# Optimization experiments

Hardware: AMD Instinct MI355X
Metric: run time of the kernel (lower is better)

## Reference

```python
import jax, jax.numpy as jnp
import numpy as np

H = 1024
V_IN = 32000
V_OUT = 32000
T = 2048
BOS, EOS = 1, 2
MAX_STEPS = 50


def setup_inputs() -> dict:
    key = jax.random.key(0)
    ks = jax.random.split(key, 10)
    def n(k, shape, scale=0.05):
        return jax.random.normal(k, shape, jnp.float32) * scale
    return {
        "src_ids": jax.random.randint(ks[0], (T,), 3, V_IN),
        "embed_input": n(ks[1], (V_IN, H), 0.1),
        "We_ih": n(ks[2], (4 * H, H)),
        "We_hh": n(ks[3], (4 * H, H)),
        "be": jnp.zeros((4 * H,), jnp.float32),
        "embed_target": n(ks[4], (V_OUT, H), 0.1),
        "Wd_ih": n(ks[5], (4 * H, H)),
        "Wd_hh": n(ks[6], (4 * H, H)),
        "bd": jnp.zeros((4 * H,), jnp.float32),
        "W_attn": n(ks[7], (H, 2 * H)),
        "b_attn": jnp.zeros((H,), jnp.float32),
        "W_out": n(ks[8], (V_OUT, H)),
        "b_out": jnp.zeros((V_OUT,), jnp.float32),
    }


def _lstm_cell(x, h, c, W_ih, W_hh, b):
    # torch LSTMCell gate order: i, f, g, o (b = b_ih + b_hh folded)
    g = W_ih @ x + W_hh @ h + b  # [4H]
    i, f, gg, o = jnp.split(g, 4)
    i = jax.nn.sigmoid(i)
    f = jax.nn.sigmoid(f)
    o = jax.nn.sigmoid(o)
    gg = jnp.tanh(gg)
    c2 = f * c + i * gg
    return o * jnp.tanh(c2), c2


def reference(src_ids, embed_input, We_ih, We_hh, be, embed_target,
              Wd_ih, Wd_hh, bd, W_attn, b_attn, W_out, b_out):
    # ---- encoder: token-wise LSTMCell scan (batch 1, state squeezed to [H]) ----
    emb = embed_input[src_ids]  # [T, H] gather (unknown-word fallback handled by in-range ids)
    h0 = jnp.zeros((H,), jnp.float32)

    def enc_step(carry, x):
        h, c = carry
        h, c = _lstm_cell(x, h, c, We_ih, We_hh, be)
        return (h, c), h

    (hT, cT), hs = jax.lax.scan(enc_step, (h0, h0), emb)  # hs: [T, H]

    # ---- greedy decoder with dot attention, fixed 50 steps + done mask ----
    def dec_step(carry, _):
        wid, ht, ct, done = carry
        x = embed_target[wid]
        ht, ct = _lstm_cell(x, ht, ct, Wd_ih, Wd_hh, bd)
        a = jax.nn.softmax(hs @ ht)          # [T] attention over encoder states
        d = a @ hs                           # [H] context
        ht_new = jnp.tanh(W_attn @ jnp.concatenate([d, ht]) + b_attn)
        logits = W_out @ ht_new + b_out      # [V_OUT]; softmax before argmax is monotone -> skip
        nid = jnp.argmax(logits).astype(wid.dtype)
        tok = jnp.where(done, 0, nid)        # pad after <eos>
        out_logits = jnp.where(done, 0.0, logits)
        done2 = done | (nid == EOS)
        return (nid, ht, ct, done2), (tok, out_logits)

    init = (jnp.asarray(BOS, src_ids.dtype), hT, cT, jnp.asarray(False))
    _, (tokens, logits) = jax.lax.scan(dec_step, init, None, length=MAX_STEPS)
    return tokens, logits  # [50], [50, V_OUT]
```

## Files before the change

kernel.cpp:

```cpp
#include <hip/hip_runtime.h>
#include <math.h>

#define HD     1024
#define TLEN   2048
#define G4H    4096
#define VOUTN  32000
#define NSTEP  50
#define BOS_ID 1
#define EOS_ID 2

#define NBLK 256
#define NTHR 256
#define JPB  (HD / NBLK)
#define TPB  (TLEN / NBLK)
#define RPB  (VOUTN / NBLK)

#define ENBLK 64
#define ENTHR 1024
#define EJPB  (HD / ENBLK)

#define SENTINEL 0xFFFFFFFFu

#define OFF_GX   ((size_t)0)
#define OFF_HS   (OFF_GX + (size_t)TLEN * G4H)
#define OFF_HD   (OFF_HS + (size_t)(TLEN + 1) * HD)
#define OFF_SC   (OFF_HD + 2 * HD)
#define OFF_DC   (OFF_SC + TLEN)
#define OFF_HTN  (OFF_DC + HD)
#define OFF_BMV  (OFF_HTN + HD)
#define OFF_BMI  (OFF_BMV + NBLK)
#define OFF_CT   (OFF_BMI + NBLK)
#define OFF_ST   (OFF_CT + HD)

#define DEV_SCOPE __HIP_MEMORY_SCOPE_AGENT

__device__ __forceinline__ float dload(const float* p) {
    return __hip_atomic_load(p, __ATOMIC_RELAXED, DEV_SCOPE);
}
__device__ __forceinline__ void dstore(float* p, float v) {
    __hip_atomic_store(p, v, __ATOMIC_RELAXED, DEV_SCOPE);
}

__global__ __launch_bounds__(256) void fill_sentinel(float* __restrict__ hsrow1)
{
    const size_t i = ((size_t)blockIdx.x * 256 + threadIdx.x) * 4;
    uint4 v = make_uint4(SENTINEL, SENTINEL, SENTINEL, SENTINEL);
    *(uint4*)(hsrow1 + i) = v;
}

__global__ __launch_bounds__(256) void gx_gemm(
    const int* __restrict__ src_ids,
    const float* __restrict__ emb,
    const float* __restrict__ Wih,
    const float* __restrict__ be,
    float* __restrict__ Gx)
{
    __shared__ float As[128][17];
    __shared__ float Bs[128][17];
    __shared__ int   sid[128];

    const int tid = threadIdx.x;
    const int t0 = blockIdx.x * 128;
    const int r0 = blockIdx.y * 128;

    if (tid < 128) sid[tid] = src_ids[t0 + tid];
    __syncthreads();

    const int tx = tid & 15;
    const int ty = tid >> 4;
    const int lrow = tid >> 1;
    const int lk   = (tid & 1) * 8;

    float acc[8][8];
#pragma unroll
    for (int i = 0; i < 8; ++i)
#pragma unroll
        for (int j = 0; j < 8; ++j) acc[i][j] = 0.f;

    for (int k0 = 0; k0 < HD; k0 += 16) {
        {
            const float* xa = emb + (size_t)sid[lrow] * HD + k0 + lk;
            float4 v0 = *(const float4*)xa;
            float4 v1 = *(const float4*)(xa + 4);
            As[lrow][lk + 0] = v0.x; As[lrow][lk + 1] = v0.y;
            As[lrow][lk + 2] = v0.z; As[lrow][lk + 3] = v0.w;
            As[lrow][lk + 4] = v1.x; As[lrow][lk + 5] = v1.y;
            As[lrow][lk + 6] = v1.z; As[lrow][lk + 7] = v1.w;
            const float* wb = Wih + (size_t)(r0 + lrow) * HD + k0 + lk;
            float4 w0 = *(const float4*)wb;
            float4 w1 = *(const float4*)(wb + 4);
            Bs[lrow][lk + 0] = w0.x; Bs[lrow][lk + 1] = w0.y;
            Bs[lrow][lk + 2] = w0.z; Bs[lrow][lk + 3] = w0.w;
            Bs[lrow][lk + 4] = w1.x; Bs[lrow][lk + 5] = w1.y;
            Bs[lrow][lk + 6] = w1.z; Bs[lrow][lk + 7] = w1.w;
        }
        __syncthreads();
#pragma unroll
        for (int kk = 0; kk < 16; ++kk) {
            float a[8], bv[8];
#pragma unroll
            for (int i = 0; i < 8; ++i) a[i]  = As[ty * 8 + i][kk];
#pragma unroll
            for (int j = 0; j < 8; ++j) bv[j] = Bs[tx * 8 + j][kk];
#pragma unroll
            for (int i = 0; i < 8; ++i)
#pragma unroll
                for (int j = 0; j < 8; ++j)
                    acc[i][j] = fmaf(a[i], bv[j], acc[i][j]);
        }
        __syncthreads();
    }

    float bev[8];
#pragma unroll
    for (int j = 0; j < 8; ++j) bev[j] = be[r0 + tx * 8 + j];
#pragma unroll
    for (int i = 0; i < 8; ++i) {
        const int t = t0 + ty * 8 + i;
        float* dst = Gx + (size_t)t * G4H + r0 + tx * 8;
#pragma unroll
        for (int j = 0; j < 8; ++j) dst[j] = acc[i][j] + bev[j];
    }
}

__global__ __launch_bounds__(1024, 4) void enc_kernel(
    const float* __restrict__ Whh,
    const float* __restrict__ Gx,
    float* __restrict__ wsf)
{
    float* hs   = wsf + OFF_HS;
    float* hd   = wsf + OFF_HD;
    float* cdec = wsf + OFF_CT;
    int*   st   = (int*)(wsf + OFF_ST);

    const int b    = blockIdx.x;
    const int tid  = threadIdx.x;
    const int w    = tid >> 6;
    const int lane = tid & 63;
    const int j0   = b * EJPB;
    const int g    = w >> 2;
    const int e0   = (w & 3) * 4;

    __shared__ float bufH[HD];
    __shared__ float g_s[64];
    __shared__ float c_s[EJPB];

    float wreg[4][16];
#pragma unroll
    for (int d = 0; d < 4; ++d) {
        const int grow = g * HD + j0 + e0 + d;
        const float* src = Whh + (size_t)grow * HD + lane;
#pragma unroll
        for (int q = 0; q < 16; ++q) wreg[d][q] = src[q * 64];
    }

    if (tid < EJPB) c_s[tid] = 0.f;

    for (int t = 0; t < TLEN; ++t) {
        {
            const float* src = hs + (size_t)t * HD + tid;
            float v = dload(src);
            while (__float_as_uint(v) == SENTINEL) {
                __builtin_amdgcn_s_sleep(1);
                v = dload(src);
            }
            bufH[tid] = v;
        }
        __syncthreads();

        float acc[4];
#pragma unroll
        for (int d = 0; d < 4; ++d) {
            float a = 0.f;
#pragma unroll
            for (int q = 0; q < 16; ++q)
                a = fmaf(wreg[d][q], bufH[q * 64 + lane], a);
#pragma unroll
            for (int off = 32; off > 0; off >>= 1) a += __shfl_down(a, off);
            acc[d] = a;
        }
        if (lane == 0) {
#pragma unroll
            for (int d = 0; d < 4; ++d) g_s[g * 16 + e0 + d] = acc[d];
        }
        __syncthreads();

        if (tid < EJPB) {
            const int j = j0 + tid;
            const float* gx = Gx + (size_t)t * G4H;
            const float gi = g_s[tid]      + gx[0 * HD + j];
            const float gf = g_s[16 + tid] + gx[1 * HD + j];
            const float gg = g_s[32 + tid] + gx[2 * HD + j];
            const float go = g_s[48 + tid] + gx[3 * HD + j];
            const float i_ = 1.f / (1.f + expf(-gi));
            const float f_ = 1.f / (1.f + expf(-gf));
            const float o_ = 1.f / (1.f + expf(-go));
            const float g2 = tanhf(gg);
            const float c2 = f_ * c_s[tid] + i_ * g2;
            c_s[tid] = c2;
            dstore(hs + (size_t)(t + 1) * HD + j, o_ * tanhf(c2));
        }
    }

    if (tid < EJPB) {
        cdec[j0 + tid] = c_s[tid];
        hd[j0 + tid]   = hs[(size_t)TLEN * HD + j0 + tid];
    }
    if (b == 0 && tid == 0) st[0] = BOS_ID;
}


__global__ __launch_bounds__(256) void k_gates(
    const float* __restrict__ embT,
    const float* __restrict__ Wdih,
    const float* __restrict__ Wdhh,
    const float* __restrict__ bdv,
    float* __restrict__ wsf, int s)
{
    float* hd   = wsf + OFF_HD;
    float* cdec = wsf + OFF_CT;
    const int* st = (const int*)(wsf + OFF_ST);

    const int b    = blockIdx.x;
    const int tid  = threadIdx.x;
    const int w    = tid >> 6;
    const int lane = tid & 63;
    const int j0   = b * JPB;

    const float* hcur = hd + (s & 1) * HD;
    float*       hnxt = hd + ((s + 1) & 1) * HD;

    __shared__ float bufAB[2 * HD];
    __shared__ float g_s[4 * JPB];
    const float4* buf4 = (const float4*)bufAB;

    const int widv = st[s] & 0xFFFF;
    const float* x = embT + (size_t)widv * HD;
    for (int i = tid; i < HD; i += NTHR) {
        bufAB[i]      = x[i];
        bufAB[HD + i] = hcur[i];
    }
    __syncthreads();

#pragma unroll
    for (int d = 0; d < 4; ++d) {
        const int grow = w * HD + j0 + d;
        const float4* wi4 = (const float4*)(Wdih + (size_t)grow * HD);
        const float4* wh4 = (const float4*)(Wdhh + (size_t)grow * HD);
        float4 a4 = make_float4(0.f, 0.f, 0.f, 0.f);
#pragma unroll
        for (int q = 0; q < 4; ++q) {
            float4 wv = wi4[q * 64 + lane], xv = buf4[q * 64 + lane];
            a4.x = fmaf(wv.x, xv.x, a4.x); a4.y = fmaf(wv.y, xv.y, a4.y);
            a4.z = fmaf(wv.z, xv.z, a4.z); a4.w = fmaf(wv.w, xv.w, a4.w);
            float4 wv2 = wh4[q * 64 + lane], hv = buf4[256 + q * 64 + lane];
            a4.x = fmaf(wv2.x, hv.x, a4.x); a4.y = fmaf(wv2.y, hv.y, a4.y);
            a4.z = fmaf(wv2.z, hv.z, a4.z); a4.w = fmaf(wv2.w, hv.w, a4.w);
        }
        float a = (a4.x + a4.y) + (a4.z + a4.w);
#pragma unroll
        for (int off = 32; off > 0; off >>= 1) a += __shfl_down(a, off);
        if (lane == 0) g_s[w * 4 + d] = a;
    }
    __syncthreads();

    if (tid < JPB) {
        const int j = j0 + tid;
        const float gi = g_s[0 * 4 + tid] + bdv[0 * HD + j];
        const float gf = g_s[1 * 4 + tid] + bdv[1 * HD + j];
        const float gg = g_s[2 * 4 + tid] + bdv[2 * HD + j];
        const float go = g_s[3 * 4 + tid] + bdv[3 * HD + j];
        const float i_ = 1.f / (1.f + expf(-gi));
        const float f_ = 1.f / (1.f + expf(-gf));
        const float o_ = 1.f / (1.f + expf(-go));
        const float g2 = tanhf(gg);
        const float c2 = f_ * cdec[j] + i_ * g2;
        cdec[j] = c2;
        hnxt[j] = o_ * tanhf(c2);
    }
}

__global__ __launch_bounds__(256) void k_scores(float* __restrict__ wsf, int s)
{
    const float* hs = wsf + OFF_HS;
    const float* hnxt = wsf + OFF_HD + (size_t)((s + 1) & 1) * HD;
    float* sc = wsf + OFF_SC;

    const int b    = blockIdx.x;
    const int tid  = threadIdx.x;
    const int w    = tid >> 6;
    const int lane = tid & 63;

    __shared__ float bufH[HD];
    const float4* buf4 = (const float4*)bufH;
    for (int i = tid; i < HD; i += NTHR) bufH[i] = hnxt[i];
    __syncthreads();

#pragma unroll
    for (int d = 0; d < 2; ++d) {
        const int t = b * TPB + w * 2 + d;
        const float4* hr4 = (const float4*)(hs + (size_t)(t + 1) * HD);
        float4 a4 = make_float4(0.f, 0.f, 0.f, 0.f);
#pragma unroll
        for (int q = 0; q < 4; ++q) {
            float4 hv = hr4[q * 64 + lane], bv = buf4[q * 64 + lane];
            a4.x = fmaf(hv.x, bv.x, a4.x); a4.y = fmaf(hv.y, bv.y, a4.y);
            a4.z = fmaf(hv.z, bv.z, a4.z); a4.w = fmaf(hv.w, bv.w, a4.w);
        }
        float a = (a4.x + a4.y) + (a4.z + a4.w);
#pragma unroll
        for (int off = 32; off > 0; off >>= 1) a += __shfl_down(a, off);
        if (lane == 0) sc[t] = a;
    }
}

__global__ __launch_bounds__(256) void k_ctx(float* __restrict__ wsf)
{
    const float* hs = wsf + OFF_HS;
    const float* sc = wsf + OFF_SC;
    float* dctx = wsf + OFF_DC;

    const int b    = blockIdx.x;
    const int tid  = threadIdx.x;
    const int w    = tid >> 6;
    const int lane = tid & 63;
    const int j0   = b * JPB;

    __shared__ float sc_s[TLEN];
    __shared__ float red[NTHR];

    for (int t = tid; t < TLEN; t += NTHR) sc_s[t] = sc[t];
    __syncthreads();

    float lm = -INFINITY;
    for (int t = tid; t < TLEN; t += NTHR) lm = fmaxf(lm, sc_s[t]);
    red[tid] = lm; __syncthreads();
    for (int s2 = NTHR / 2; s2 > 0; s2 >>= 1) {
        if (tid < s2) red[tid] = fmaxf(red[tid], red[tid + s2]);
        __syncthreads();
    }
    const float m = red[0]; __syncthreads();
    float lz = 0.f;
    for (int t = tid; t < TLEN; t += NTHR) lz += expf(sc_s[t] - m);
    red[tid] = lz; __syncthreads();
    for (int s2 = NTHR / 2; s2 > 0; s2 >>= 1) {
        if (tid < s2) red[tid] += red[tid + s2];
        __syncthreads();
    }
    const float Zi = 1.f / red[0]; __syncthreads();

    const int j = j0 + w;
    float a = 0.f;
#pragma unroll
    for (int it = 0; it < TLEN / 64; ++it) {
        const int t = lane + it * 64;
        const float wt = expf(sc_s[t] - m) * Zi;
        a = fmaf(wt, hs[(size_t)(t + 1) * HD + j], a);
    }
#pragma unroll
    for (int off = 32; off > 0; off >>= 1) a += __shfl_down(a, off);
    if (lane == 0) dctx[j] = a;
}

__global__ __launch_bounds__(256) void k_attn(
    const float* __restrict__ Wattn,
    const float* __restrict__ battn,
    float* __restrict__ wsf, int s)
{
    const float* dctx = wsf + OFF_DC;
    const float* hnxt = wsf + OFF_HD + (size_t)((s + 1) & 1) * HD;
    float* htn = wsf + OFF_HTN;

    const int b    = blockIdx.x;
    const int tid  = threadIdx.x;
    const int w    = tid >> 6;
    const int lane = tid & 63;
    const int j0   = b * JPB;

    __shared__ float bufAB[2 * HD];
    const float4* buf4 = (const float4*)bufAB;
    for (int i = tid; i < HD; i += NTHR) {
        bufAB[i]      = dctx[i];
        bufAB[HD + i] = hnxt[i];
    }
    __syncthreads();

    const int j = j0 + w;
    const float4* wr4 = (const float4*)(Wattn + (size_t)j * (2 * HD));
    float4 a4 = make_float4(0.f, 0.f, 0.f, 0.f);
#pragma unroll
    for (int q = 0; q < 8; ++q) {
        float4 wv = wr4[q * 64 + lane], bv = buf4[q * 64 + lane];
        a4.x = fmaf(wv.x, bv.x, a4.x); a4.y = fmaf(wv.y, bv.y, a4.y);
        a4.z = fmaf(wv.z, bv.z, a4.z); a4.w = fmaf(wv.w, bv.w, a4.w);
    }
    float a = (a4.x + a4.y) + (a4.z + a4.w);
#pragma unroll
    for (int off = 32; off > 0; off >>= 1) a += __shfl_down(a, off);
    if (lane == 0) htn[j] = tanhf(a + battn[j]);
}

__global__ __launch_bounds__(256) void k_logits(
    const float* __restrict__ Wout,
    const float* __restrict__ bout,
    float* __restrict__ wsf,
    float* __restrict__ out, int s)
{
    const float* htn = wsf + OFF_HTN;
    float* bmv = wsf + OFF_BMV;
    int*   bmi = (int*)(wsf + OFF_BMI);
    const int* st = (const int*)(wsf + OFF_ST);

    const int b    = blockIdx.x;
    const int tid  = threadIdx.x;
    const int w    = tid >> 6;
    const int lane = tid & 63;

    __shared__ float bufH[HD];
    __shared__ float red[4];
    __shared__ int   redi[4];
    const float4* buf4 = (const float4*)bufH;

    const int donev = (st[s] >> 16) & 1;
    for (int i = tid; i < HD; i += NTHR) bufH[i] = htn[i];
    __syncthreads();

    const int r0b = b * RPB;
    const int rbeg = r0b + w * 32;
    const int rend = min(r0b + RPB, rbeg + 32);
    float bv = -INFINITY; int bi = 0x7fffffff;
    for (int r = rbeg; r < rend; r += 2) {
        const int two = (r + 1 < rend);
        const float4* w0 = (const float4*)(Wout + (size_t)r * HD);
        const float4* w1 = (const float4*)(Wout + (size_t)(r + two) * HD);
        float4 a04 = make_float4(0.f, 0.f, 0.f, 0.f);
        float4 a14 = make_float4(0.f, 0.f, 0.f, 0.f);
#pragma unroll
        for (int q = 0; q < 4; ++q) {
            float4 hv = buf4[q * 64 + lane];
            float4 x0 = w0[q * 64 + lane];
            float4 x1 = w1[q * 64 + lane];
            a04.x = fmaf(x0.x, hv.x, a04.x); a04.y = fmaf(x0.y, hv.y, a04.y);
            a04.z = fmaf(x0.z, hv.z, a04.z); a04.w = fmaf(x0.w, hv.w, a04.w);
            a14.x = fmaf(x1.x, hv.x, a14.x); a14.y = fmaf(x1.y, hv.y, a14.y);
            a14.z = fmaf(x1.z, hv.z, a14.z); a14.w = fmaf(x1.w, hv.w, a14.w);
        }
        float a0 = (a04.x + a04.y) + (a04.z + a04.w);
        float a1 = (a14.x + a14.y) + (a14.z + a14.w);
#pragma unroll
        for (int off = 32; off > 0; off >>= 1) {
            a0 += __shfl_down(a0, off);
            a1 += __shfl_down(a1, off);
        }
        if (lane == 0) {
            a0 += bout[r];
            out[NSTEP + (size_t)s * VOUTN + r] = donev ? 0.f : a0;
            if (a0 > bv) { bv = a0; bi = r; }
            if (two) {
                a1 += bout[r + 1];
                out[NSTEP + (size_t)s * VOUTN + r + 1] = donev ? 0.f : a1;
                if (a1 > bv) { bv = a1; bi = r + 1; }
            }
        }
    }
    if (lane == 0) { red[w] = bv; redi[w] = bi; }
    __syncthreads();
    if (tid == 0) {
        float v = red[0]; int ii = redi[0];
#pragma unroll
        for (int q = 1; q < 4; ++q)
            if (red[q] > v || (red[q] == v && redi[q] < ii)) { v = red[q]; ii = redi[q]; }
        bmv[b] = v; bmi[b] = ii;
    }
}

__global__ __launch_bounds__(256) void k_amax(
    float* __restrict__ wsf, float* __restrict__ out, int s)
{
    const float* bmv = wsf + OFF_BMV;
    const int*   bmi = (const int*)(wsf + OFF_BMI);
    int* st = (int*)(wsf + OFF_ST);

    const int tid = threadIdx.x;
    __shared__ float red[NTHR];
    __shared__ int   redi[NTHR];

    red[tid] = bmv[tid]; redi[tid] = bmi[tid];
    __syncthreads();
    for (int s2 = NTHR / 2; s2 > 0; s2 >>= 1) {
        if (tid < s2) {
            if (red[tid + s2] > red[tid] ||
                (red[tid + s2] == red[tid] && redi[tid + s2] < redi[tid])) {
                red[tid] = red[tid + s2]; redi[tid] = redi[tid + s2];
            }
        }
        __syncthreads();
    }
    if (tid == 0) {
        const int nid = redi[0];
        const int donev = (st[s] >> 16) & 1;
        out[s] = donev ? 0.f : (float)nid;
        const int done2 = donev | (nid == EOS_ID);
        st[s + 1] = (done2 << 16) | nid;
    }
}

extern "C" void kernel_launch(void* const* d_in, const int* in_sizes, int n_in,
                              void* d_out, int out_size, void* d_ws, size_t ws_size,
                              hipStream_t stream) {
    (void)in_sizes; (void)n_in; (void)out_size; (void)ws_size;
    const int*   src_ids = (const int*)  d_in[0];
    const float* emb_in  = (const float*)d_in[1];
    const float* We_ih   = (const float*)d_in[2];
    const float* We_hh   = (const float*)d_in[3];
    const float* be      = (const float*)d_in[4];
    const float* emb_tgt = (const float*)d_in[5];
    const float* Wd_ih   = (const float*)d_in[6];
    const float* Wd_hh   = (const float*)d_in[7];
    const float* bd      = (const float*)d_in[8];
    const float* W_attn  = (const float*)d_in[9];
    const float* b_attn  = (const float*)d_in[10];
    const float* W_out   = (const float*)d_in[11];
    const float* b_out   = (const float*)d_in[12];

    float* outp = (float*)d_out;
    float* wsf  = (float*)d_ws;

    hipMemsetAsync(wsf + OFF_HS, 0, HD * sizeof(float), stream);
    fill_sentinel<<<TLEN, 256, 0, stream>>>(wsf + OFF_HS + HD);

    dim3 g1(TLEN / 128, G4H / 128);
    gx_gemm<<<g1, 256, 0, stream>>>(src_ids, emb_in, We_ih, be, wsf + OFF_GX);

    {
        const float* a_Whh = We_hh;
        const float* a_Gx  = wsf + OFF_GX;
        float* a_ws  = wsf;
        void* args[] = { &a_Whh, &a_Gx, &a_ws };
        hipLaunchCooperativeKernel(reinterpret_cast<void*>(enc_kernel),
                                   dim3(ENBLK), dim3(ENTHR), args, 0, stream);
    }

    for (int s = 0; s < NSTEP; ++s) {
        k_gates <<<NBLK, NTHR, 0, stream>>>(emb_tgt, Wd_ih, Wd_hh, bd, wsf, s);
        k_scores<<<NBLK, NTHR, 0, stream>>>(wsf, s);
        k_ctx   <<<NBLK, NTHR, 0, stream>>>(wsf);
        k_attn  <<<NBLK, NTHR, 0, stream>>>(W_attn, b_attn, wsf, s);
        k_logits<<<NBLK, NTHR, 0, stream>>>(W_out, b_out, wsf, outp, s);
        k_amax  <<<1,    NTHR, 0, stream>>>(wsf, outp, s);
    }
}
```

Before: 10.30 ms.

## Fuse argmax into gates kernel, transpose encoder states, widen logits grid

The per-step single-block argmax kernel is removed. Every gates block now redoes the final argmax reduction over the logits partials, and block 0 writes the token and done state. The encoder states are transposed once after the encoder so the context reduction reads contiguous rows, and the logits kernel is spread over 500 blocks with a fixed 16 rows per wave. The encoder kernel also prefetches its input-gate slice into shared memory, and the softmax uses fast exp. This trades 50 kernel launches and strided reads for redundant reductions and an extra 8MB buffer.

```diff
diff --git a/kernel.cpp b/kernel.cpp
--- a/kernel.cpp
+++ b/kernel.cpp
@@ -1,4 +1,5 @@
 #include <hip/hip_runtime.h>
+#include <hip/hip_cooperative_groups.h>
 #include <math.h>
 
 #define HD     1024
@@ -9,11 +10,12 @@
 #define BOS_ID 1
 #define EOS_ID 2
 
-#define NBLK 256
-#define NTHR 256
-#define JPB  (HD / NBLK)
-#define TPB  (TLEN / NBLK)
-#define RPB  (VOUTN / NBLK)
+#define NBLK   256
+#define NTHR   256
+#define JPB    (HD / NBLK)
+#define TPB    (TLEN / NBLK)
+#define NBLK_L 500
+#define RPW_L  16
 
 #define ENBLK 64
 #define ENTHR 1024
@@ -28,9 +30,11 @@
 #define OFF_DC   (OFF_SC + TLEN)
 #define OFF_HTN  (OFF_DC + HD)
 #define OFF_BMV  (OFF_HTN + HD)
-#define OFF_BMI  (OFF_BMV + NBLK)
-#define OFF_CT   (OFF_BMI + NBLK)
+#define OFF_BMI  (OFF_BMV + 512)
+#define OFF_CT   (OFF_BMI + 512)
 #define OFF_ST   (OFF_CT + HD)
+#define OFF_HST  (OFF_ST + 64)
+#define WS_NEED_HST ((OFF_HST + (size_t)HD * TLEN) * sizeof(float))
 
 #define DEV_SCOPE __HIP_MEMORY_SCOPE_AGENT
 
@@ -144,6 +148,7 @@
     __shared__ float bufH[HD];
     __shared__ float g_s[64];
     __shared__ float c_s[EJPB];
+    __shared__ float gxbuf[64];
 
     float wreg[4][16];
 #pragma unroll
@@ -168,6 +173,13 @@
         }
         __syncthreads();
 
+        if (tid >= 64 && tid < 128) {
+            const int idx = tid - 64;
+            const int gg2 = idx >> 4;
+            const int ee  = idx & 15;
+            gxbuf[idx] = Gx[(size_t)t * G4H + gg2 * HD + j0 + ee];
+        }
+
         float acc[4];
 #pragma unroll
         for (int d = 0; d < 4; ++d) {
@@ -187,11 +199,10 @@
 
         if (tid < EJPB) {
             const int j = j0 + tid;
-            const float* gx = Gx + (size_t)t * G4H;
-            const float gi = g_s[tid]      + gx[0 * HD + j];
-            const float gf = g_s[16 + tid] + gx[1 * HD + j];
-            const float gg = g_s[32 + tid] + gx[2 * HD + j];
-            const float go = g_s[48 + tid] + gx[3 * HD + j];
+            const float gi = g_s[tid]      + gxbuf[tid];
+            const float gf = g_s[16 + tid] + gxbuf[16 + tid];
+            const float gg = g_s[32 + tid] + gxbuf[32 + tid];
+            const float go = g_s[48 + tid] + gxbuf[48 + tid];
             const float i_ = 1.f / (1.f + expf(-gi));
             const float f_ = 1.f / (1.f + expf(-gf));
             const float o_ = 1.f / (1.f + expf(-go));
@@ -209,17 +220,40 @@
     if (b == 0 && tid == 0) st[0] = BOS_ID;
 }
 
+__global__ __launch_bounds__(256) void k_transpose(
+    const float* __restrict__ hs, float* __restrict__ hsT)
+{
+    __shared__ float tile[32][33];
+    const int t0  = blockIdx.x * 32;
+    const int j0b = blockIdx.y * 32;
+    const int tx  = threadIdx.x & 31;
+    const int ty  = threadIdx.x >> 5;
+#pragma unroll
+    for (int k = 0; k < 4; ++k) {
+        const int trow = t0 + ty + k * 8;
+        tile[ty + k * 8][tx] = hs[(size_t)(trow + 1) * HD + j0b + tx];
+    }
+    __syncthreads();
+#pragma unroll
+    for (int k = 0; k < 4; ++k) {
+        const int j = j0b + ty + k * 8;
+        hsT[(size_t)j * TLEN + t0 + tx] = tile[tx][ty + k * 8];
+    }
+}
 
 __global__ __launch_bounds__(256) void k_gates(
     const float* __restrict__ embT,
     const float* __restrict__ Wdih,
     const float* __restrict__ Wdhh,
     const float* __restrict__ bdv,
-    float* __restrict__ wsf, int s)
+    float* __restrict__ wsf,
+    float* __restrict__ out, int s)
 {
     float* hd   = wsf + OFF_HD;
     float* cdec = wsf + OFF_CT;
-    const int* st = (const int*)(wsf + OFF_ST);
+    int*   st   = (int*)(wsf + OFF_ST);
+    const float* bmv = wsf + OFF_BMV;
+    const int*   bmi = (const int*)(wsf + OFF_BMI);
 
     const int b    = blockIdx.x;
     const int tid  = threadIdx.x;
@@ -232,16 +266,51 @@
 
     __shared__ float bufAB[2 * HD];
     __shared__ float g_s[4 * JPB];
+    __shared__ float rv[NTHR];
+    __shared__ int   ri[NTHR];
+    __shared__ int   s_wid;
+
+    for (int i = tid; i < HD; i += NTHR) bufAB[HD + i] = hcur[i];
+
+    if (s == 0) {
+        if (tid == 0) s_wid = st[0] & 0xFFFF;
+        __syncthreads();
+    } else {
+        float v1 = bmv[tid]; int i1 = bmi[tid];
+        if (tid + 256 < NBLK_L) {
+            float v2 = bmv[tid + 256]; int i2 = bmi[tid + 256];
+            if (v2 > v1 || (v2 == v1 && i2 < i1)) { v1 = v2; i1 = i2; }
+        }
+        rv[tid] = v1; ri[tid] = i1;
+        __syncthreads();
+        for (int s2 = 128; s2 > 0; s2 >>= 1) {
+            if (tid < s2) {
+                if (rv[tid + s2] > rv[tid] ||
+                    (rv[tid + s2] == rv[tid] && ri[tid + s2] < ri[tid])) {
+                    rv[tid] = rv[tid + s2]; ri[tid] = ri[tid + s2];
+                }
+            }
+            __syncthreads();
+        }
+        if (tid == 0) {
+            const int nid   = ri[0];
+            const int prev  = st[s - 1];
+            const int dprev = (prev >> 16) & 1;
+            const int dnew  = dprev | (nid == EOS_ID);
+            s_wid = nid;
+            if (b == 0) {
+                out[s - 1] = dprev ? 0.f : (float)nid;
+                st[s] = (dnew << 16) | nid;
+            }
+        }
+        __syncthreads();
+    }
+
+    const float* x = embT + (size_t)s_wid * HD;
+    for (int i = tid; i < HD; i += NTHR) bufAB[i] = x[i];
+    __syncthreads();
+
     const float4* buf4 = (const float4*)bufAB;
-
-    const int widv = st[s] & 0xFFFF;
-    const float* x = embT + (size_t)widv * HD;
-    for (int i = tid; i < HD; i += NTHR) {
-        bufAB[i]      = x[i];
-        bufAB[HD + i] = hcur[i];
-    }
-    __syncthreads();
-
 #pragma unroll
     for (int d = 0; d < 4; ++d) {
         const int grow = w * HD + j0 + d;
@@ -314,7 +383,8 @@
     }
 }
 
-__global__ __launch_bounds__(256) void k_ctx(float* __restrict__ wsf)
+__global__ __launch_bounds__(256) void k_ctx(
+    float* __restrict__ wsf, const float* __restrict__ hsT)
 {
     const float* hs = wsf + OFF_HS;
     const float* sc = wsf + OFF_SC;
@@ -341,7 +411,7 @@
     }
     const float m = red[0]; __syncthreads();
     float lz = 0.f;
-    for (int t = tid; t < TLEN; t += NTHR) lz += expf(sc_s[t] - m);
+    for (int t = tid; t < TLEN; t += NTHR) lz += __expf(sc_s[t] - m);
     red[tid] = lz; __syncthreads();
     for (int s2 = NTHR / 2; s2 > 0; s2 >>= 1) {
         if (tid < s2) red[tid] += red[tid + s2];
@@ -351,11 +421,19 @@
 
     const int j = j0 + w;
     float a = 0.f;
-#pragma unroll
-    for (int it = 0; it < TLEN / 64; ++it) {
-        const int t = lane + it * 64;
-        const float wt = expf(sc_s[t] - m) * Zi;
-        a = fmaf(wt, hs[(size_t)(t + 1) * HD + j], a);
+    if (hsT) {
+        const float* row = hsT + (size_t)j * TLEN;
+#pragma unroll
+        for (int it = 0; it < TLEN / 64; ++it) {
+            const int t = lane + it * 64;
+            a = fmaf(__expf(sc_s[t] - m) * Zi, row[t], a);
+        }
+    } else {
+#pragma unroll
+        for (int it = 0; it < TLEN / 64; ++it) {
+            const int t = lane + it * 64;
+            a = fmaf(__expf(sc_s[t] - m) * Zi, hs[(size_t)(t + 1) * HD + j], a);
+        }
     }
 #pragma unroll
     for (int off = 32; off > 0; off >>= 1) a += __shfl_down(a, off);
@@ -425,14 +503,11 @@
     for (int i = tid; i < HD; i += NTHR) bufH[i] = htn[i];
     __syncthreads();
 
-    const int r0b = b * RPB;
-    const int rbeg = r0b + w * 32;
-    const int rend = min(r0b + RPB, rbeg + 32);
+    const int rbeg = b * 64 + w * RPW_L;
     float bv = -INFINITY; int bi = 0x7fffffff;
-    for (int r = rbeg; r < rend; r += 2) {
-        const int two = (r + 1 < rend);
+    for (int r = rbeg; r < rbeg + RPW_L; r += 2) {
         const float4* w0 = (const float4*)(Wout + (size_t)r * HD);
-        const float4* w1 = (const float4*)(Wout + (size_t)(r + two) * HD);
+        const float4* w1 = (const float4*)(Wout + (size_t)(r + 1) * HD);
         float4 a04 = make_float4(0.f, 0.f, 0.f, 0.f);
         float4 a14 = make_float4(0.f, 0.f, 0.f, 0.f);
 #pragma unroll
@@ -454,13 +529,11 @@
         }
         if (lane == 0) {
             a0 += bout[r];
-            out[NSTEP + (size_t)s * VOUTN + r] = donev ? 0.f : a0;
+            a1 += bout[r + 1];
+            out[NSTEP + (size_t)s * VOUTN + r]     = donev ? 0.f : a0;
+            out[NSTEP + (size_t)s * VOUTN + r + 1] = donev ? 0.f : a1;
             if (a0 > bv) { bv = a0; bi = r; }
-            if (two) {
-                a1 += bout[r + 1];
-                out[NSTEP + (size_t)s * VOUTN + r + 1] = donev ? 0.f : a1;
-                if (a1 > bv) { bv = a1; bi = r + 1; }
-            }
+            if (a1 > bv) { bv = a1; bi = r + 1; }
         }
     }
     if (lane == 0) { red[w] = bv; redi[w] = bi; }
@@ -474,20 +547,25 @@
     }
 }
 
-__global__ __launch_bounds__(256) void k_amax(
-    float* __restrict__ wsf, float* __restrict__ out, int s)
+__global__ __launch_bounds__(256) void k_amax_final(
+    float* __restrict__ wsf, float* __restrict__ out)
 {
     const float* bmv = wsf + OFF_BMV;
     const int*   bmi = (const int*)(wsf + OFF_BMI);
-    int* st = (int*)(wsf + OFF_ST);
+    const int*   st  = (const int*)(wsf + OFF_ST);
 
     const int tid = threadIdx.x;
     __shared__ float red[NTHR];
     __shared__ int   redi[NTHR];
 
-    red[tid] = bmv[tid]; redi[tid] = bmi[tid];
-    __syncthreads();
-    for (int s2 = NTHR / 2; s2 > 0; s2 >>= 1) {
+    float v1 = bmv[tid]; int i1 = bmi[tid];
+    if (tid + 256 < NBLK_L) {
+        float v2 = bmv[tid + 256]; int i2 = bmi[tid + 256];
+        if (v2 > v1 || (v2 == v1 && i2 < i1)) { v1 = v2; i1 = i2; }
+    }
+    red[tid] = v1; redi[tid] = i1;
+    __syncthreads();
+    for (int s2 = 128; s2 > 0; s2 >>= 1) {
         if (tid < s2) {
             if (red[tid + s2] > red[tid] ||
                 (red[tid + s2] == red[tid] && redi[tid + s2] < redi[tid])) {
@@ -497,18 +575,16 @@
         __syncthreads();
     }
     if (tid == 0) {
-        const int nid = redi[0];
-        const int donev = (st[s] >> 16) & 1;
-        out[s] = donev ? 0.f : (float)nid;
-        const int done2 = donev | (nid == EOS_ID);
-        st[s + 1] = (done2 << 16) | nid;
+        const int nid   = redi[0];
+        const int donev = (st[NSTEP - 1] >> 16) & 1;
+        out[NSTEP - 1] = donev ? 0.f : (float)nid;
     }
 }
 
 extern "C" void kernel_launch(void* const* d_in, const int* in_sizes, int n_in,
                               void* d_out, int out_size, void* d_ws, size_t ws_size,
                               hipStream_t stream) {
-    (void)in_sizes; (void)n_in; (void)out_size; (void)ws_size;
+    (void)in_sizes; (void)n_in; (void)out_size;
     const int*   src_ids = (const int*)  d_in[0];
     const float* emb_in  = (const float*)d_in[1];
     const float* We_ih   = (const float*)d_in[2];
@@ -526,6 +602,9 @@
     float* outp = (float*)d_out;
     float* wsf  = (float*)d_ws;
 
+    const bool use_hsT = (ws_size >= WS_NEED_HST);
+    const float* hsTp = use_hsT ? (wsf + OFF_HST) : nullptr;
+
     hipMemsetAsync(wsf + OFF_HS, 0, HD * sizeof(float), stream);
     fill_sentinel<<<TLEN, 256, 0, stream>>>(wsf + OFF_HS + HD);
 
@@ -541,12 +620,16 @@
                                    dim3(ENBLK), dim3(ENTHR), args, 0, stream);
     }
 
+    if (use_hsT)
+        k_transpose<<<dim3(TLEN / 32, HD / 32), 256, 0, stream>>>(
+            wsf + OFF_HS, wsf + OFF_HST);
+
     for (int s = 0; s < NSTEP; ++s) {
-        k_gates <<<NBLK, NTHR, 0, stream>>>(emb_tgt, Wd_ih, Wd_hh, bd, wsf, s);
-        k_scores<<<NBLK, NTHR, 0, stream>>>(wsf, s);
-        k_ctx   <<<NBLK, NTHR, 0, stream>>>(wsf);
-        k_attn  <<<NBLK, NTHR, 0, stream>>>(W_attn, b_attn, wsf, s);
-        k_logits<<<NBLK, NTHR, 0, stream>>>(W_out, b_out, wsf, outp, s);
-        k_amax  <<<1,    NTHR, 0, stream>>>(wsf, outp, s);
-    }
-}
+        k_gates <<<NBLK,   NTHR, 0, stream>>>(emb_tgt, Wd_ih, Wd_hh, bd, wsf, outp, s);
+        k_scores<<<NBLK,   NTHR, 0, stream>>>(wsf, s);
+        k_ctx   <<<NBLK,   NTHR, 0, stream>>>(wsf, hsTp);
+        k_attn  <<<NBLK,   NTHR, 0, stream>>>(W_attn, b_attn, wsf, s);
+        k_logits<<<NBLK_L, NTHR, 0, stream>>>(W_out, b_out, wsf, outp, s);
+    }
+    k_amax_final<<<1, NTHR, 0, stream>>>(wsf, outp);
+}
```

Result: faster. 8.522 ms (-17.2%).
